# Optimization experiments

Hardware: AMD Instinct MI355X
Metric: run time of the kernel (lower is better)

Reference implementation:

```python
import jax, jax.numpy as jnp
import numpy as np

# ---- instant-ngp style multi-resolution hash-grid config (matches torch-ngp HashEncoder) ----
NUM_LEVELS = 16
LEVEL_DIM = 2
BASE_RES = 16
DESIRED_RES = 2048
LOG2_T = 19
T_MAX = 2 ** LOG2_T
_pls = np.exp2(np.log2(DESIRED_RES / BASE_RES) / (NUM_LEVELS - 1))  # per-level scale ~1.3819
RESOLUTIONS = [int(np.ceil(BASE_RES * _pls ** l)) for l in range(NUM_LEVELS)]
LEVEL_SIZES = [min(T_MAX, int(np.ceil((r + 1) ** 3 / 8) * 8)) for r in RESOLUTIONS]
OFFSETS = np.concatenate([[0], np.cumsum(LEVEL_SIZES)]).astype(np.int64)
TOTAL_PARAMS = int(OFFSETS[-1])
HASHED = [(r + 1) ** 3 > T_MAX for r in RESOLUTIONS]
CORNERS = np.array([[i, j, k] for i in (0, 1) for j in (0, 1) for k in (0, 1)], dtype=np.float32)  # [8,3]

N_POINTS = 524288
MULTIRES = 6  # positional embedding freqs -> input_ch = 3 + 3*2*6 = 39
D_IN0 = 3 + MULTIRES * 6 + NUM_LEVELS * LEVEL_DIM  # 71


def hash_encode(x, table):
    """x: [N,3] in [0,1]; table: [TOTAL_PARAMS, LEVEL_DIM] -> [N, NUM_LEVELS*LEVEL_DIM]."""
    cn = jnp.asarray(CORNERS)              # [8,3]
    cn_u = cn.astype(jnp.uint32)
    p1, p2, p3 = jnp.uint32(1), jnp.uint32(2654435761), jnp.uint32(805459861)
    outs = []
    for l in range(NUM_LEVELS):
        res = RESOLUTIONS[l]
        pos = x * jnp.float32(res - 1)     # [N,3]
        p0 = jnp.floor(pos)
        w = pos - p0                        # [N,3] trilinear fractions
        cpos = p0.astype(jnp.uint32)[:, None, :] + cn_u[None]  # [N,8,3] corner coords
        if HASHED[l]:
            idx = (cpos[..., 0] * p1) ^ (cpos[..., 1] * p2) ^ (cpos[..., 2] * p3)
            idx = (idx % jnp.uint32(LEVEL_SIZES[l])).astype(jnp.int32)
        else:
            stride = jnp.uint32(res + 1)
            idx = (cpos[..., 0] + cpos[..., 1] * stride + cpos[..., 2] * stride * stride).astype(jnp.int32)
        feats = table[int(OFFSETS[l]) + idx]  # [N,8,LEVEL_DIM] irregular gather
        cw = jnp.where(cn[None] == 1.0, w[:, None, :], 1.0 - w[:, None, :])  # [N,8,3]
        wgt = cw[..., 0] * cw[..., 1] * cw[..., 2]  # [N,8]
        outs.append(jnp.einsum('nc,ncd->nd', wgt, feats))  # [N,LEVEL_DIM]
    return jnp.concatenate(outs, axis=-1)


def pos_embed(x):
    # NeRF embedder, include_input=True, log-sampled freqs 2^0..2^(MULTIRES-1), sin/cos
    freqs = jnp.asarray(2.0 ** np.arange(MULTIRES), dtype=x.dtype)   # [6]
    ang = x[:, None, :] * freqs[None, :, None]                        # [N,6,3]
    sc = jnp.stack([jnp.sin(ang), jnp.cos(ang)], axis=2)              # [N,6,2,3]
    return jnp.concatenate([x, sc.reshape(x.shape[0], -1)], axis=-1)  # [N,39]


def linear_wn(x, v, g, b):
    # nn.utils.weight_norm: W = g * v / ||v||_row
    Wn = v * (g / jnp.linalg.norm(v, axis=1))[:, None]
    return x @ Wn.T + b


def softplus100(x):
    # nn.Softplus(beta=100)
    return jax.nn.softplus(100.0 * x) * 0.01


def setup_inputs() -> dict:
    key = jax.random.key(0)
    ks = jax.random.split(key, 8)
    x = jax.random.uniform(ks[0], (N_POINTS, 3), dtype=jnp.float32)
    hash_table = jax.random.uniform(ks[1], (TOTAL_PARAMS, LEVEL_DIM), jnp.float32, -1e-4, 1e-4)

    def lin(k, dout, din):
        v = jax.random.normal(k, (dout, din), jnp.float32) * jnp.float32(np.sqrt(2.0 / dout))
        g = jnp.linalg.norm(v, axis=1)  # weight_norm init: g = ||v||
        b = jnp.zeros((dout,), jnp.float32)
        return v, g, b

    v0, g0, b0 = lin(ks[2], 256, D_IN0)   # 71 -> 256
    v1, g1, b1 = lin(ks[3], 256, 256)     # 256 -> 256
    v2, g2, b2 = lin(ks[4], 257, 256)     # 256 -> 1 + feature_vector_size
    return {"x": x, "hash_table": hash_table,
            "v0": v0, "g0": g0, "b0": b0,
            "v1": v1, "g1": g1, "b1": b1,
            "v2": v2, "g2": g2, "b2": b2}


def reference(x, hash_table, v0, g0, b0, v1, g1, b1, v2, g2, b2):
    # ImplicitNetworkGrid.forward (divide_factor = 1.0, use_grid_feature = True)
    feat = hash_encode(x, hash_table)                    # [N,32]
    h = jnp.concatenate([pos_embed(x), feat], axis=-1)   # [N,71] = cat(embed, feature)
    h = softplus100(linear_wn(h, v0, g0, b0))
    h = softplus100(linear_wn(h, v1, g1, b1))
    return linear_wn(h, v2, g2, b2)                      # [N,257]: sdf + feature vector
```

## Files before the change

### kernel.cpp

```cpp
#include <hip/hip_runtime.h>
#include <cmath>

typedef float f32x4 __attribute__((ext_vector_type(4)));
typedef short short8 __attribute__((ext_vector_type(8)));

#define N_POINTS 524288
#define TMASK 0x7FFFFu
#define NCELLS 32768

struct HashCfg { int res[16]; int off[16]; unsigned hashed_mask; int total; };

#define S0_OFF   0
#define S1_OFF   1024
#define S2_OFF   2048
#define W2L_OFF  3328
#define B0_OFF   4608
#define B1_OFF   (B0_OFF + 49152)
#define B2_OFF   (B1_OFF + 131072)
#define TBF_OFF  (B2_OFF + 131072)

__device__ inline unsigned short f2bf(float f){
  unsigned u = __float_as_uint(f);
  u = (u + 0x7FFFu + ((u >> 16) & 1u)) >> 16;
  return (unsigned short)u;
}
__device__ inline float bf2f(unsigned short h){
  return __uint_as_float(((unsigned)h) << 16);
}
__device__ inline float softplus100_fast(float x){
  float y = 100.f * x;
  return 0.01f * (fmaxf(y, 0.f) + __logf(1.f + __expf(-fabsf(y))));
}
__device__ inline unsigned morton5(unsigned cx, unsigned cy, unsigned cz){
  unsigned k = 0;
  #pragma unroll
  for (int b = 0; b < 5; b++){
    k |= ((cx >> b) & 1u) << (3*b)
       | ((cy >> b) & 1u) << (3*b + 1)
       | ((cz >> b) & 1u) << (3*b + 2);
  }
  return k;
}

__global__ void scale_kernel(const float* __restrict__ v0, const float* __restrict__ g0,
                             const float* __restrict__ v1, const float* __restrict__ g1,
                             const float* __restrict__ v2, const float* __restrict__ g2,
                             char* __restrict__ ws){
  int r = blockIdx.x * 256 + threadIdx.x;
  if (r < 256){
    float s = 0.f;
    for (int k = 0; k < 71; k++){ float t = v0[r*71+k]; s += t*t; }
    ((float*)(ws + S0_OFF))[r] = g0[r] / sqrtf(s);
  } else if (r < 512){
    int o = r - 256; float s = 0.f;
    for (int k = 0; k < 256; k++){ float t = v1[o*256+k]; s += t*t; }
    ((float*)(ws + S1_OFF))[o] = g1[o] / sqrtf(s);
  } else if (r < 769){
    int o = r - 512; float s = 0.f;
    for (int k = 0; k < 256; k++){ float t = v2[o*256+k]; s += t*t; }
    ((float*)(ws + S2_OFF))[o] = g2[o] / sqrtf(s);
  }
}

__global__ void pack_kernel(const float* __restrict__ v0, const float* __restrict__ v1,
                            const float* __restrict__ v2, char* __restrict__ ws){
  int i = blockIdx.x * 256 + threadIdx.x;
  const float* s0 = (const float*)(ws + S0_OFF);
  const float* s1 = (const float*)(ws + S1_OFF);
  const float* s2 = (const float*)(ws + S2_OFF);
  if (i < 24576){
    int j = i & 7, l = (i >> 3) & 63, q = i >> 9;
    int kt = q % 3, nt = q / 3;
    int k = kt*32 + (l >> 4)*8 + j, col = nt*16 + (l & 15);
    float v = (k < 71) ? v0[col*71 + k] * s0[col] : 0.f;
    ((unsigned short*)(ws + B0_OFF))[i] = f2bf(v);
  } else if (i < 90112){
    int e = i - 24576;
    int j = e & 7, l = (e >> 3) & 63, q = e >> 9;
    int kt = q & 7, nt = q >> 3;
    int k = kt*32 + (l >> 4)*8 + j, col = nt*16 + (l & 15);
    ((unsigned short*)(ws + B1_OFF))[e] = f2bf(v1[col*256 + k] * s1[col]);
  } else if (i < 155648){
    int e = i - 90112;
    int j = e & 7, l = (e >> 3) & 63, q = e >> 9;
    int kt = q & 7, nt = q >> 3;
    int k = kt*32 + (l >> 4)*8 + j, col = nt*16 + (l & 15);
    ((unsigned short*)(ws + B2_OFF))[e] = f2bf(v2[col*256 + k] * s2[col]);
  } else if (i < 155904){
    int k = i - 155648;
    ((float*)(ws + W2L_OFF))[k] = v2[256*256 + k] * s2[256];
  }
}

__global__ void tconv_kernel(const float* __restrict__ table, char* __restrict__ ws, int total){
  int i = blockIdx.x * 256 + threadIdx.x;
  if (i < total){
    float2 v = ((const float2*)table)[i];
    ((unsigned*)(ws + TBF_OFF))[i] = ((unsigned)f2bf(v.x)) | (((unsigned)f2bf(v.y)) << 16);
  }
}

__global__ void hist_kernel(const float* __restrict__ xin,
                            unsigned* __restrict__ hist, unsigned* __restrict__ keys){
  int i = blockIdx.x * 256 + threadIdx.x;
  float x0 = xin[i*3], x1 = xin[i*3+1], x2 = xin[i*3+2];
  unsigned cx = min(31u, (unsigned)(x0 * 32.f));
  unsigned cy = min(31u, (unsigned)(x1 * 32.f));
  unsigned cz = min(31u, (unsigned)(x2 * 32.f));
  unsigned k = morton5(cx, cy, cz);
  keys[i] = k;
  atomicAdd(&hist[k], 1u);
}

__global__ __launch_bounds__(1024) void scan_kernel(unsigned* __restrict__ hist){
  __shared__ unsigned sdata[1024];
  int t = threadIdx.x;
  unsigned loc[32];
  unsigned s = 0;
  #pragma unroll
  for (int k = 0; k < 32; k++){ loc[k] = hist[t*32 + k]; s += loc[k]; }
  sdata[t] = s;
  __syncthreads();
  for (int d = 1; d < 1024; d <<= 1){
    unsigned v = (t >= d) ? sdata[t - d] : 0u;
    __syncthreads();
    sdata[t] += v;
    __syncthreads();
  }
  unsigned run = (t == 0) ? 0u : sdata[t - 1];
  #pragma unroll
  for (int k = 0; k < 32; k++){ unsigned c = loc[k]; hist[t*32 + k] = run; run += c; }
}

__global__ void scatter_kernel(const float* __restrict__ xin,
                               const unsigned* __restrict__ keys,
                               unsigned* __restrict__ hist, int* __restrict__ perm,
                               float* __restrict__ sx){
  int i = blockIdx.x * 256 + threadIdx.x;
  unsigned k = keys[i];
  unsigned r = atomicAdd(&hist[k], 1u);
  perm[r] = i;
  sx[r*3]   = xin[i*3];
  sx[r*3+1] = xin[i*3+1];
  sx[r*3+2] = xin[i*3+2];
}

template<int USEBF>
__global__ __launch_bounds__(512, 4) void fused7(
    const float* __restrict__ xin, const float* __restrict__ table,
    char* __restrict__ ws, const int* __restrict__ perm, const float* __restrict__ sx,
    const float* __restrict__ b0, const float* __restrict__ b1, const float* __restrict__ b2,
    float* __restrict__ out, HashCfg cfg)
{
  __shared__ unsigned short buf[128 * 256];
  __shared__ float colsc[4][128];
  __shared__ int pids_sh[128];

  const int tid  = threadIdx.x;
  const int p    = tid & 127;
  const int lgrp = tid >> 7;
  const int grp  = tid >> 6;
  const int wm   = grp >> 2;
  const int wn   = grp & 3;
  const int l    = tid & 63;
  const int lr   = l & 15;
  const int lh   = l >> 4;
  const int lb   = (blockIdx.x & 7) * 512 + (blockIdx.x >> 3);
  const int base_idx = lb * 128;

  const unsigned* __restrict__ tbf = (const unsigned*)(ws + TBF_OFF);
  const short8* B0p = (const short8*)(ws + B0_OFF);
  const short8* B1p = (const short8*)(ws + B1_OFF);
  const short8* B2p = (const short8*)(ws + B2_OFF);
  const float* w2l = (const float*)(ws + W2L_OFF);

  auto stB = [&](int row, int col, float v){
    buf[row*256 + (col ^ ((row & 7) << 3))] = f2bf(v);
  };
  auto ldB = [&](int row, int kb) -> short8 {
    return *(const short8*)&buf[row*256 + (kb ^ ((row & 7) << 3))];
  };

  if (tid < 128) pids_sh[tid] = perm ? perm[base_idx + tid] : (base_idx + tid);

  {
    const float* src = sx ? sx : xin;
    const float X = src[(base_idx + p)*3];
    const float Y = src[(base_idx + p)*3 + 1];
    const float Z = src[(base_idx + p)*3 + 2];

    unsigned vb[4][8];
    float2   vf2[4][8];

    #pragma unroll
    for (int ii = 0; ii < 4; ii++){
      int lev = lgrp*4 + ii;
      int res = cfg.res[lev];
      float scl = (float)(res - 1);
      unsigned cx0 = (unsigned)floorf(X*scl);
      unsigned cy0 = (unsigned)floorf(Y*scl);
      unsigned cz0 = (unsigned)floorf(Z*scl);
      unsigned r1 = (unsigned)(res + 1);
      bool hl = (cfg.hashed_mask >> lev) & 1;
      unsigned base = (unsigned)cfg.off[lev];
      #pragma unroll
      for (int c = 0; c < 8; c++){
        unsigned bx = (c >> 2) & 1, by = (c >> 1) & 1, bz = c & 1;
        unsigned cx = cx0 + bx, cy = cy0 + by, cz = cz0 + bz;
        unsigned hidx = hl ? ((cx ^ (cy * 2654435761u) ^ (cz * 805459861u)) & TMASK)
                           : (cx + cy * r1 + cz * r1 * r1);
        if constexpr (USEBF) vb[ii][c]  = tbf[base + hidx];
        else                 vf2[ii][c] = *(const float2*)(table + (size_t)(base + hidx) * 2u);
      }
    }

    if (lgrp < 3){
      float xv[3] = {X, Y, Z};
      #pragma unroll
      for (int fi = 0; fi < 2; fi++){
        int f = lgrp*2 + fi;
        float fr = (float)(1 << f);
        #pragma unroll
        for (int d = 0; d < 3; d++){
          float ang = xv[d] * fr;
          stB(p, 3 + f*6 + d,     __sinf(ang));
          stB(p, 3 + f*6 + 3 + d, __cosf(ang));
        }
      }
    } else {
      stB(p, 0, X); stB(p, 1, Y); stB(p, 2, Z);
      #pragma unroll
      for (int c = 71; c < 96; c++)
        buf[p*256 + (c ^ ((p & 7) << 3))] = 0;
    }

    #pragma unroll
    for (int ii = 0; ii < 4; ii++){
      int lev = lgrp*4 + ii;
      int res = cfg.res[lev];
      float scl = (float)(res - 1);
      float px = X*scl, py = Y*scl, pz = Z*scl;
      float wx = px - floorf(px), wy = py - floorf(py), wz = pz - floorf(pz);
      float f0 = 0.f, f1 = 0.f;
      #pragma unroll
      for (int c = 0; c < 8; c++){
        unsigned bx = (c >> 2) & 1, by = (c >> 1) & 1, bz = c & 1;
        float w = (bx ? wx : 1.f - wx) * (by ? wy : 1.f - wy) * (bz ? wz : 1.f - wz);
        if constexpr (USEBF){
          unsigned u = vb[ii][c];
          f0 += w * __uint_as_float(u << 16);
          f1 += w * __uint_as_float(u & 0xffff0000u);
        } else {
          f0 += w * vf2[ii][c].x;
          f1 += w * vf2[ii][c].y;
        }
      }
      stB(p, 39 + 2*lev, f0);
      stB(p, 40 + 2*lev, f1);
    }
  }
  __syncthreads();

  auto hidden_layer = [&](const short8* Bp, int nkt, const float* bias){
    f32x4 acc[4][4];
    #pragma unroll
    for (int a = 0; a < 4; a++)
      #pragma unroll
      for (int b = 0; b < 4; b++) acc[a][b] = (f32x4){0.f,0.f,0.f,0.f};
    __builtin_amdgcn_s_setprio(1);
    for (int kt = 0; kt < nkt; kt++){
      short8 af[4];
      #pragma unroll
      for (int mt = 0; mt < 4; mt++) af[mt] = ldB(wm*64 + mt*16 + lr, kt*32 + lh*8);
      #pragma unroll
      for (int nt = 0; nt < 4; nt++){
        short8 bf = Bp[((wn*4 + nt)*nkt + kt)*64 + l];
        #pragma unroll
        for (int mt = 0; mt < 4; mt++)
          acc[mt][nt] = __builtin_amdgcn_mfma_f32_16x16x32_bf16(af[mt], bf, acc[mt][nt], 0, 0, 0);
      }
    }
    __builtin_amdgcn_s_setprio(0);
    __syncthreads();
    float bb[4];
    #pragma unroll
    for (int nt = 0; nt < 4; nt++) bb[nt] = bias[wn*64 + nt*16 + lr];
    #pragma unroll
    for (int mt = 0; mt < 4; mt++)
      #pragma unroll
      for (int nt = 0; nt < 4; nt++){
        int c = wn*64 + nt*16 + lr;
        #pragma unroll
        for (int j = 0; j < 4; j++)
          stB(wm*64 + mt*16 + lh*4 + j, c, softplus100_fast(acc[mt][nt][j] + bb[nt]));
      }
  };

  hidden_layer(B0p, 3, b0);
  __syncthreads();
  hidden_layer(B1p, 8, b1);
  __syncthreads();

  {
    int row = tid & 127, ch = tid >> 7;
    float s = 0.f;
    #pragma unroll
    for (int q = 0; q < 8; q++){
      short8 h = ldB(row, ch*64 + q*8);
      #pragma unroll
      for (int j = 0; j < 8; j++)
        s += bf2f((unsigned short)h[j]) * w2l[ch*64 + q*8 + j];
    }
    colsc[ch][row] = s;
  }

  {
    f32x4 acc[4][4];
    #pragma unroll
    for (int a = 0; a < 4; a++)
      #pragma unroll
      for (int b = 0; b < 4; b++) acc[a][b] = (f32x4){0.f,0.f,0.f,0.f};
    __builtin_amdgcn_s_setprio(1);
    for (int kt = 0; kt < 8; kt++){
      short8 af[4];
      #pragma unroll
      for (int mt = 0; mt < 4; mt++) af[mt] = ldB(wm*64 + mt*16 + lr, kt*32 + lh*8);
      #pragma unroll
      for (int nt = 0; nt < 4; nt++){
        short8 bf = B2p[((wn*4 + nt)*8 + kt)*64 + l];
        #pragma unroll
        for (int mt = 0; mt < 4; mt++)
          acc[mt][nt] = __builtin_amdgcn_mfma_f32_16x16x32_bf16(af[mt], bf, acc[mt][nt], 0, 0, 0);
      }
    }
    __builtin_amdgcn_s_setprio(0);
    __syncthreads();
    float bb[4];
    #pragma unroll
    for (int nt = 0; nt < 4; nt++) bb[nt] = b2[wn*64 + nt*16 + lr];
    #pragma unroll
    for (int mt = 0; mt < 4; mt++)
      #pragma unroll
      for (int nt = 0; nt < 4; nt++){
        int c = wn*64 + nt*16 + lr;
        #pragma unroll
        for (int j = 0; j < 4; j++)
          out[(size_t)pids_sh[wm*64 + mt*16 + lh*4 + j]*257 + c] = acc[mt][nt][j] + bb[nt];
      }
    if (tid < 128)
      out[(size_t)pids_sh[tid]*257 + 256] =
        colsc[0][tid] + colsc[1][tid] + colsc[2][tid] + colsc[3][tid] + b2[256];
  }
}

static HashCfg make_cfg(){
  HashCfg c;
  double pls = exp2(log2(2048.0 / 16.0) / 15.0);
  long long off = 0;
  unsigned mask = 0;
  for (int l = 0; l < 16; l++){
    int r = (int)ceil(16.0 * pow(pls, (double)l));
    c.res[l] = r;
    c.off[l] = (int)off;
    double n3 = (double)(r + 1) * (double)(r + 1) * (double)(r + 1);
    long long size;
    if (n3 > 524288.0){ mask |= (1u << l); }
    size = (long long)(ceil(n3 / 8.0) * 8.0);
    if (size > 524288) size = 524288;
    off += size;
  }
  c.hashed_mask = mask;
  c.total = (int)off;
  return c;
}

extern "C" void kernel_launch(void* const* d_in, const int* in_sizes, int n_in,
                              void* d_out, int out_size, void* d_ws, size_t ws_size,
                              hipStream_t stream) {
  const float* x     = (const float*)d_in[0];
  const float* table = (const float*)d_in[1];
  const float* v0 = (const float*)d_in[2];
  const float* g0 = (const float*)d_in[3];
  const float* b0 = (const float*)d_in[4];
  const float* v1 = (const float*)d_in[5];
  const float* g1 = (const float*)d_in[6];
  const float* b1 = (const float*)d_in[7];
  const float* v2 = (const float*)d_in[8];
  const float* g2 = (const float*)d_in[9];
  const float* b2 = (const float*)d_in[10];
  float* out = (float*)d_out;
  char* ws = (char*)d_ws;

  HashCfg cfg = make_cfg();
  size_t tbf_bytes = (size_t)cfg.total * 4u;
  size_t hist_off  = (TBF_OFF + tbf_bytes + 255) & ~(size_t)255;
  size_t keys_off  = hist_off + (size_t)NCELLS * 4;
  size_t perm_off  = keys_off + (size_t)N_POINTS * 4;
  size_t sx_off    = perm_off + (size_t)N_POINTS * 4;
  size_t need_sort = sx_off + (size_t)N_POINTS * 12;
  size_t need_bf   = TBF_OFF + tbf_bytes;

  hipLaunchKernelGGL(scale_kernel, dim3(4), dim3(256), 0, stream, v0, g0, v1, g1, v2, g2, ws);
  hipLaunchKernelGGL(pack_kernel, dim3(609), dim3(256), 0, stream, v0, v1, v2, ws);

  const int nblk = N_POINTS / 128;

  if (ws_size >= need_sort){
    unsigned* hist = (unsigned*)(ws + hist_off);
    unsigned* keys = (unsigned*)(ws + keys_off);
    int*      perm = (int*)(ws + perm_off);
    float*    sx   = (float*)(ws + sx_off);
    hipMemsetAsync(hist, 0, (size_t)NCELLS * 4, stream);
    hipLaunchKernelGGL(tconv_kernel, dim3((cfg.total + 255) / 256), dim3(256), 0, stream,
                       table, ws, cfg.total);
    hipLaunchKernelGGL(hist_kernel, dim3(N_POINTS / 256), dim3(256), 0, stream, x, hist, keys);
    hipLaunchKernelGGL(scan_kernel, dim3(1), dim3(1024), 0, stream, hist);
    hipLaunchKernelGGL(scatter_kernel, dim3(N_POINTS / 256), dim3(256), 0, stream,
                       x, keys, hist, perm, sx);
    hipLaunchKernelGGL((fused7<1>), dim3(nblk), dim3(512), 0, stream,
                       x, table, ws, perm, sx, b0, b1, b2, out, cfg);
  } else if (ws_size >= need_bf){
    hipLaunchKernelGGL(tconv_kernel, dim3((cfg.total + 255) / 256), dim3(256), 0, stream,
                       table, ws, cfg.total);
    hipLaunchKernelGGL((fused7<1>), dim3(nblk), dim3(512), 0, stream,
                       x, table, ws, (const int*)nullptr, (const float*)nullptr,
                       b0, b1, b2, out, cfg);
  } else {
    hipLaunchKernelGGL((fused7<0>), dim3(nblk), dim3(512), 0, stream,
                       x, table, ws, (const int*)nullptr, (const float*)nullptr,
                       b0, b1, b2, out, cfg);
  }
}
```

Baseline: 787.5 us.

## Stage coarse hash-grid levels per block in shared memory via bounding-box region

Each block computes the bounding box of its (spatially sorted) points, then cooperatively loads the grid cells covering that box for the six coarsest levels into a shared-memory region. The trilinear interpolation for those levels then reads from LDS instead of issuing eight scattered global loads per level per point. This adds extra barriers, a block-wide reduction, integer index decode for the cooperative load, and 4 KB more shared memory, which could hurt occupancy. Levels whose region exceeds the capacity fall back to global gathers.

```diff
diff --git a/kernel.cpp b/kernel.cpp
--- a/kernel.cpp
+++ b/kernel.cpp
@@ -7,6 +7,9 @@
 #define N_POINTS 524288
 #define TMASK 0x7FFFFu
 #define NCELLS 32768
+#define P2H 2654435761u
+#define P3H 805459861u
+#define RGN_CAP 1024
 
 struct HashCfg { int res[16]; int off[16]; unsigned hashed_mask; int total; };
 
@@ -146,7 +149,7 @@
 }
 
 template<int USEBF>
-__global__ __launch_bounds__(512, 4) void fused7(
+__global__ __launch_bounds__(512, 4) void fused9(
     const float* __restrict__ xin, const float* __restrict__ table,
     char* __restrict__ ws, const int* __restrict__ perm, const float* __restrict__ sx,
     const float* __restrict__ b0, const float* __restrict__ b1, const float* __restrict__ b2,
@@ -155,6 +158,9 @@
   __shared__ unsigned short buf[128 * 256];
   __shared__ float colsc[4][128];
   __shared__ int pids_sh[128];
+  __shared__ unsigned rgn[RGN_CAP];
+  __shared__ int rprm[6][10];
+  __shared__ int bboxi[6];
 
   const int tid  = threadIdx.x;
   const int p    = tid & 127;
@@ -182,19 +188,59 @@
   };
 
   if (tid < 128) pids_sh[tid] = perm ? perm[base_idx + tid] : (base_idx + tid);
+  if (tid < 6)   bboxi[tid] = (tid & 1) ? 0 : 0x7f7fffff;
+
+  const float* src = sx ? sx : xin;
+  const float X = src[(base_idx + p)*3];
+  const float Y = src[(base_idx + p)*3 + 1];
+  const float Z = src[(base_idx + p)*3 + 2];
+  __syncthreads();
 
   {
-    const float* src = sx ? sx : xin;
-    const float X = src[(base_idx + p)*3];
-    const float Y = src[(base_idx + p)*3 + 1];
-    const float Z = src[(base_idx + p)*3 + 2];
-
-    unsigned vb[4][8];
-    float2   vf2[4][8];
-
-    #pragma unroll
-    for (int ii = 0; ii < 4; ii++){
-      int lev = lgrp*4 + ii;
+    float mnx = X, mxx = X, mny = Y, mxy = Y, mnz = Z, mxz = Z;
+    #pragma unroll
+    for (int m = 1; m < 64; m <<= 1){
+      mnx = fminf(mnx, __shfl_xor(mnx, m)); mxx = fmaxf(mxx, __shfl_xor(mxx, m));
+      mny = fminf(mny, __shfl_xor(mny, m)); mxy = fmaxf(mxy, __shfl_xor(mxy, m));
+      mnz = fminf(mnz, __shfl_xor(mnz, m)); mxz = fmaxf(mxz, __shfl_xor(mxz, m));
+    }
+    if (l == 0){
+      atomicMin(&bboxi[0], __float_as_int(mnx)); atomicMax(&bboxi[1], __float_as_int(mxx));
+      atomicMin(&bboxi[2], __float_as_int(mny)); atomicMax(&bboxi[3], __float_as_int(mxy));
+      atomicMin(&bboxi[4], __float_as_int(mnz)); atomicMax(&bboxi[5], __float_as_int(mxz));
+    }
+  }
+  __syncthreads();
+
+  if (tid == 0){
+    float mnx = __int_as_float(bboxi[0]), mxx = __int_as_float(bboxi[1]);
+    float mny = __int_as_float(bboxi[2]), mxy = __int_as_float(bboxi[3]);
+    float mnz = __int_as_float(bboxi[4]), mxz = __int_as_float(bboxi[5]);
+    int off = 0;
+    for (int lev = 0; lev < 6; lev++){
+      float scl = (float)(cfg.res[lev] - 1);
+      int x0 = (int)floorf(mnx*scl), x1 = (int)floorf(mxx*scl);
+      int y0 = (int)floorf(mny*scl), y1 = (int)floorf(mxy*scl);
+      int z0 = (int)floorf(mnz*scl), z1 = (int)floorf(mxz*scl);
+      int dx = x1 - x0 + 2, dy = y1 - y0 + 2, dz = z1 - z0 + 2;
+      int cnt = dx * dy * dz;
+      int ok = (off + cnt <= RGN_CAP) ? 1 : 0;
+      rprm[lev][0] = x0; rprm[lev][1] = y0; rprm[lev][2] = z0;
+      rprm[lev][3] = dx; rprm[lev][4] = dx*dy; rprm[lev][5] = off; rprm[lev][6] = ok;
+      rprm[lev][7] = __float_as_int(1.0f / (float)dx);
+      rprm[lev][8] = __float_as_int(1.0f / (float)(dx*dy));
+      rprm[lev][9] = cnt;
+      if (ok) off += cnt;
+    }
+  }
+  __syncthreads();
+
+  unsigned vb[4][8];
+  float2   vf2[4][8];
+  #pragma unroll
+  for (int ii = 0; ii < 4; ii++){
+    int lev = lgrp*4 + ii;
+    if (lev >= 6){
       int res = cfg.res[lev];
       float scl = (float)(res - 1);
       unsigned cx0 = (unsigned)floorf(X*scl);
@@ -207,41 +253,106 @@
       for (int c = 0; c < 8; c++){
         unsigned bx = (c >> 2) & 1, by = (c >> 1) & 1, bz = c & 1;
         unsigned cx = cx0 + bx, cy = cy0 + by, cz = cz0 + bz;
-        unsigned hidx = hl ? ((cx ^ (cy * 2654435761u) ^ (cz * 805459861u)) & TMASK)
+        unsigned hidx = hl ? ((cx ^ (cy * P2H) ^ (cz * P3H)) & TMASK)
                            : (cx + cy * r1 + cz * r1 * r1);
         if constexpr (USEBF) vb[ii][c]  = tbf[base + hidx];
         else                 vf2[ii][c] = *(const float2*)(table + (size_t)(base + hidx) * 2u);
       }
     }
-
-    if (lgrp < 3){
-      float xv[3] = {X, Y, Z};
-      #pragma unroll
-      for (int fi = 0; fi < 2; fi++){
-        int f = lgrp*2 + fi;
-        float fr = (float)(1 << f);
-        #pragma unroll
-        for (int d = 0; d < 3; d++){
-          float ang = xv[d] * fr;
-          stB(p, 3 + f*6 + d,     __sinf(ang));
-          stB(p, 3 + f*6 + 3 + d, __cosf(ang));
+  }
+
+  if constexpr (USEBF){
+    for (int lev = 0; lev < 6; lev++){
+      if (!rprm[lev][6]) continue;
+      int dx  = rprm[lev][3], dxy = rprm[lev][4], off = rprm[lev][5], cnt = rprm[lev][9];
+      float invdx  = __int_as_float(rprm[lev][7]);
+      float invdxy = __int_as_float(rprm[lev][8]);
+      int ox = rprm[lev][0], oy = rprm[lev][1], oz = rprm[lev][2];
+      int res = cfg.res[lev];
+      unsigned r1 = (unsigned)(res + 1);
+      bool hl = (cfg.hashed_mask >> lev) & 1;
+      unsigned base = (unsigned)cfg.off[lev];
+      for (int e = tid; e < cnt; e += 512){
+        int k = (int)((float)e * invdxy);
+        if ((k+1)*dxy <= e) k++;
+        if (k*dxy > e) k--;
+        int rem = e - k*dxy;
+        int j = (int)((float)rem * invdx);
+        if ((j+1)*dx <= rem) j++;
+        if (j*dx > rem) j--;
+        int i = rem - j*dx;
+        unsigned gx = (unsigned)(ox + i), gy = (unsigned)(oy + j), gz = (unsigned)(oz + k);
+        unsigned hidx = hl ? ((gx ^ (gy * P2H) ^ (gz * P3H)) & TMASK)
+                           : (gx + gy * r1 + gz * r1 * r1);
+        rgn[off + e] = tbf[base + hidx];
+      }
+    }
+  }
+
+  if (lgrp < 3){
+    float xv[3] = {X, Y, Z};
+    #pragma unroll
+    for (int fi = 0; fi < 2; fi++){
+      int f = lgrp*2 + fi;
+      float fr = (float)(1 << f);
+      #pragma unroll
+      for (int d = 0; d < 3; d++){
+        float ang = xv[d] * fr;
+        stB(p, 3 + f*6 + d,     __sinf(ang));
+        stB(p, 3 + f*6 + 3 + d, __cosf(ang));
+      }
+    }
+  } else {
+    stB(p, 0, X); stB(p, 1, Y); stB(p, 2, Z);
+    #pragma unroll
+    for (int c = 71; c < 96; c++)
+      buf[p*256 + (c ^ ((p & 7) << 3))] = 0;
+  }
+  __syncthreads();
+
+  #pragma unroll
+  for (int ii = 0; ii < 4; ii++){
+    int lev = lgrp*4 + ii;
+    int res = cfg.res[lev];
+    float scl = (float)(res - 1);
+    float px = X*scl, py = Y*scl, pz = Z*scl;
+    float fx = floorf(px), fy = floorf(py), fz = floorf(pz);
+    float wx = px - fx, wy = py - fy, wz = pz - fz;
+    float f0 = 0.f, f1 = 0.f;
+    if (lev < 6 && USEBF && rprm[lev][6]){
+      int dx  = rprm[lev][3], dxy = rprm[lev][4], off = rprm[lev][5];
+      int bidx = off + ((int)fx - rprm[lev][0]) + ((int)fy - rprm[lev][1])*dx
+               + ((int)fz - rprm[lev][2])*dxy;
+      #pragma unroll
+      for (int c = 0; c < 8; c++){
+        int bx = (c >> 2) & 1, by = (c >> 1) & 1, bz = c & 1;
+        float w = (bx ? wx : 1.f - wx) * (by ? wy : 1.f - wy) * (bz ? wz : 1.f - wz);
+        unsigned u = rgn[bidx + bx + by*dx + bz*dxy];
+        f0 += w * __uint_as_float(u << 16);
+        f1 += w * __uint_as_float(u & 0xffff0000u);
+      }
+    } else if (lev < 6){
+      unsigned cx0 = (unsigned)fx, cy0 = (unsigned)fy, cz0 = (unsigned)fz;
+      unsigned r1 = (unsigned)(res + 1);
+      bool hl = (cfg.hashed_mask >> lev) & 1;
+      unsigned base = (unsigned)cfg.off[lev];
+      #pragma unroll
+      for (int c = 0; c < 8; c++){
+        unsigned bx = (c >> 2) & 1, by = (c >> 1) & 1, bz = c & 1;
+        unsigned cx = cx0 + bx, cy = cy0 + by, cz = cz0 + bz;
+        unsigned hidx = hl ? ((cx ^ (cy * P2H) ^ (cz * P3H)) & TMASK)
+                           : (cx + cy * r1 + cz * r1 * r1);
+        float w = (bx ? wx : 1.f - wx) * (by ? wy : 1.f - wy) * (bz ? wz : 1.f - wz);
+        if constexpr (USEBF){
+          unsigned u = tbf[base + hidx];
+          f0 += w * __uint_as_float(u << 16);
+          f1 += w * __uint_as_float(u & 0xffff0000u);
+        } else {
+          float2 fv = *(const float2*)(table + (size_t)(base + hidx) * 2u);
+          f0 += w * fv.x; f1 += w * fv.y;
         }
       }
     } else {
-      stB(p, 0, X); stB(p, 1, Y); stB(p, 2, Z);
-      #pragma unroll
-      for (int c = 71; c < 96; c++)
-        buf[p*256 + (c ^ ((p & 7) << 3))] = 0;
-    }
-
-    #pragma unroll
-    for (int ii = 0; ii < 4; ii++){
-      int lev = lgrp*4 + ii;
-      int res = cfg.res[lev];
-      float scl = (float)(res - 1);
-      float px = X*scl, py = Y*scl, pz = Z*scl;
-      float wx = px - floorf(px), wy = py - floorf(py), wz = pz - floorf(pz);
-      float f0 = 0.f, f1 = 0.f;
       #pragma unroll
       for (int c = 0; c < 8; c++){
         unsigned bx = (c >> 2) & 1, by = (c >> 1) & 1, bz = c & 1;
@@ -255,9 +366,9 @@
           f1 += w * vf2[ii][c].y;
         }
       }
-      stB(p, 39 + 2*lev, f0);
-      stB(p, 40 + 2*lev, f1);
-    }
+    }
+    stB(p, 39 + 2*lev, f0);
+    stB(p, 40 + 2*lev, f1);
   }
   __syncthreads();
 
@@ -417,16 +528,16 @@
     hipLaunchKernelGGL(scan_kernel, dim3(1), dim3(1024), 0, stream, hist);
     hipLaunchKernelGGL(scatter_kernel, dim3(N_POINTS / 256), dim3(256), 0, stream,
                        x, keys, hist, perm, sx);
-    hipLaunchKernelGGL((fused7<1>), dim3(nblk), dim3(512), 0, stream,
+    hipLaunchKernelGGL((fused9<1>), dim3(nblk), dim3(512), 0, stream,
                        x, table, ws, perm, sx, b0, b1, b2, out, cfg);
   } else if (ws_size >= need_bf){
     hipLaunchKernelGGL(tconv_kernel, dim3((cfg.total + 255) / 256), dim3(256), 0, stream,
                        table, ws, cfg.total);
-    hipLaunchKernelGGL((fused7<1>), dim3(nblk), dim3(512), 0, stream,
+    hipLaunchKernelGGL((fused9<1>), dim3(nblk), dim3(512), 0, stream,
                        x, table, ws, (const int*)nullptr, (const float*)nullptr,
                        b0, b1, b2, out, cfg);
   } else {
-    hipLaunchKernelGGL((fused7<0>), dim3(nblk), dim3(512), 0, stream,
+    hipLaunchKernelGGL((fused9<0>), dim3(nblk), dim3(512), 0, stream,
                        x, table, ws, (const int*)nullptr, (const float*)nullptr,
                        b0, b1, b2, out, cfg);
   }
```

After: 828.8 us. 1.05x slower.
